# Optimization experiments

Measured on AMD Instinct MI355X. Metric: run time of the kernel, lower is better.

Reference implementation:

```python
import jax, jax.numpy as jnp
import numpy as np

RMS_EPS = 1e-6


def setup_inputs() -> dict:
    key = jax.random.key(0)
    ks = jax.random.split(key, 6)
    B, S, D, F, E = 4, 2048, 1024, 4096, 8
    scale = 0.02
    return {
        "hidden_states": jax.random.normal(ks[0], (B, S, D), dtype=jnp.float32),
        "norm_weight": jnp.ones((D,), dtype=jnp.float32),
        "gate_w": jax.random.normal(ks[1], (E, D), dtype=jnp.float32) * scale,
        "w1": jax.random.normal(ks[2], (E, D, F), dtype=jnp.float32) * scale,
        "w3": jax.random.normal(ks[3], (E, D, F), dtype=jnp.float32) * scale,
        "w2": jax.random.normal(ks[4], (E, F, D), dtype=jnp.float32) * scale,
        "top_k": 2,
    }


def reference(hidden_states, norm_weight, gate_w, w1, w3, w2, top_k):
    B, S, D = hidden_states.shape
    E = gate_w.shape[0]
    # norm_fn: RMSNorm (pre-MoE norm in Mixtral block)
    x = hidden_states * jax.lax.rsqrt(jnp.mean(jnp.square(hidden_states), axis=-1, keepdims=True) + RMS_EPS)
    x = (x * norm_weight).reshape(-1, D)  # [T, D], T = B*S
    # router
    router_logits = jnp.einsum('td,ed->te', x, gate_w)  # [T, E]
    routing = jax.nn.softmax(router_logits.astype(jnp.float32), axis=-1)
    top_w, top_idx = jax.lax.top_k(routing, top_k)  # [T, k]
    top_w = top_w / jnp.sum(top_w, axis=-1, keepdims=True)
    top_w = top_w.astype(x.dtype)
    # dense-masked expert combine: tokens not routed to expert e get weight 0,
    # mathematically identical to the gather/scatter loop in the original.
    out = jnp.zeros_like(x)
    for e in range(E):  # fixed small loop over experts
        w_e = jnp.sum(jnp.where(top_idx == e, top_w, 0.0), axis=-1)  # [T]
        h = jax.nn.silu(x @ w1[e]) * (x @ w3[e])  # [T, F] SwiGLU expert
        out = out + w_e[:, None] * (h @ w2[e])
    return out.reshape(B, S, D), router_logits
```

## Files before the change

kernel.cpp:

```cpp
#include <hip/hip_runtime.h>
#include <hip/hip_bf16.h>

#define T_TOK 8192
#define D_DIM 1024
#define F_DIM 4096
#define E_NUM 8

typedef short s16x8 __attribute__((ext_vector_type(8)));
typedef float f32x4 __attribute__((ext_vector_type(4)));
typedef unsigned short u16x8 __attribute__((ext_vector_type(8)));

__device__ __forceinline__ unsigned short f2bf(float f) {
  union { float f; unsigned int u; } v; v.f = f;
  unsigned int u = v.u;
  return (unsigned short)((u + 0x7FFFu + ((u >> 16) & 1u)) >> 16);
}

__device__ __forceinline__ void async16(const void* g, void* l) {
  __builtin_amdgcn_global_load_lds((const __attribute__((address_space(1))) void*)g,
                                   (__attribute__((address_space(3))) void*)l, 16, 0, 0);
}

__global__ __launch_bounds__(256) void prepass_kernel(
    const float* __restrict__ hs, const float* __restrict__ nw,
    const float* __restrict__ gw, const float* __restrict__ w1,
    const float* __restrict__ w3, const float* __restrict__ w2,
    unsigned short* __restrict__ xb, unsigned short* __restrict__ w13t,
    unsigned short* __restrict__ w2t, float* __restrict__ logits_out,
    int* __restrict__ cnt, int* __restrict__ ilist, float* __restrict__ wlist) {
  __shared__ unsigned short tileS[64][72];
  __shared__ float red[4];
  __shared__ float pl[4][8];
  int bx = blockIdx.x;
  int tid = threadIdx.x;
  if (bx < 24576) {
    int tensor = bx >> 13;
    int e = (bx >> 10) & 7;
    int tl = bx & 1023;
    const float* src; int C, tr, tc;
    if (tensor == 0) {
      src = w1 + (size_t)e * D_DIM * F_DIM; C = F_DIM; tr = tl >> 6; tc = tl & 63;
    } else if (tensor == 1) {
      src = w3 + (size_t)e * D_DIM * F_DIM; C = F_DIM; tr = tl >> 6; tc = tl & 63;
    } else {
      src = w2 + (size_t)e * F_DIM * D_DIM; C = D_DIM; tr = tl >> 4; tc = tl & 15;
    }
    int r0 = tr * 64, c0 = tc * 64;
    int rr = tid >> 4, ccb = (tid & 15) * 4;
#pragma unroll
    for (int i = 0; i < 4; ++i) {
      int r = rr + i * 16;
      float4 v = *(const float4*)(src + (size_t)(r0 + r) * C + c0 + ccb);
      tileS[ccb + 0][r] = f2bf(v.x);
      tileS[ccb + 1][r] = f2bf(v.y);
      tileS[ccb + 2][r] = f2bf(v.z);
      tileS[ccb + 3][r] = f2bf(v.w);
    }
    __syncthreads();
    int row = tid >> 2, col = (tid & 3) * 16;
    unsigned short* dp;
    if (tensor < 2) {
      int f = c0 + row;
      int prow = ((f >> 5) * 64) + (f & 31) + (tensor == 1 ? 32 : 0);
      dp = w13t + ((size_t)e * 8192 + prow) * D_DIM + r0 + col;
    } else {
      dp = w2t + ((size_t)e * D_DIM + c0 + row) * F_DIM + r0 + col;
    }
    u16x8 v0, v1;
#pragma unroll
    for (int j = 0; j < 8; ++j) { v0[j] = tileS[row][col + j]; v1[j] = tileS[row][col + 8 + j]; }
    *(u16x8*)dp = v0;
    *(u16x8*)(dp + 8) = v1;
  } else {
    int t = bx - 24576;
    int lane = tid & 63, wid = tid >> 6;
    float4 v = ((const float4*)(hs + (size_t)t * D_DIM))[tid];
    float ss = v.x * v.x + v.y * v.y + v.z * v.z + v.w * v.w;
#pragma unroll
    for (int o = 32; o > 0; o >>= 1) ss += __shfl_xor(ss, o);
    if (lane == 0) red[wid] = ss;
    __syncthreads();
    float ms = (red[0] + red[1] + red[2] + red[3]) * (1.0f / 1024.0f);
    float rs = rsqrtf(ms + 1e-6f);
    float4 wv = ((const float4*)nw)[tid];
    float x0 = v.x * rs * wv.x, x1 = v.y * rs * wv.y;
    float x2 = v.z * rs * wv.z, x3 = v.w * rs * wv.w;
    ((ushort4*)(xb + (size_t)t * D_DIM))[tid] =
        make_ushort4(f2bf(x0), f2bf(x1), f2bf(x2), f2bf(x3));
    float p[8];
#pragma unroll
    for (int e = 0; e < 8; ++e) {
      float4 g = ((const float4*)(gw + (size_t)e * D_DIM))[tid];
      p[e] = x0 * g.x + x1 * g.y + x2 * g.z + x3 * g.w;
    }
#pragma unroll
    for (int e = 0; e < 8; ++e) {
#pragma unroll
      for (int o = 32; o > 0; o >>= 1) p[e] += __shfl_xor(p[e], o);
    }
    if (lane == 0) {
#pragma unroll
      for (int e = 0; e < 8; ++e) pl[wid][e] = p[e];
    }
    __syncthreads();
    if (tid == 0) {
      float l[8];
#pragma unroll
      for (int e = 0; e < 8; ++e) {
        l[e] = pl[0][e] + pl[1][e] + pl[2][e] + pl[3][e];
        logits_out[(size_t)t * 8 + e] = l[e];
      }
      int i0 = 0; float b0 = l[0];
#pragma unroll
      for (int e = 1; e < 8; ++e) if (l[e] > b0) { b0 = l[e]; i0 = e; }
      int i1 = (i0 == 0) ? 1 : 0; float b1 = l[i1];
#pragma unroll
      for (int e = 0; e < 8; ++e) if (e != i0 && l[e] > b1) { b1 = l[e]; i1 = e; }
      float wa = 1.0f / (1.0f + __expf(b1 - b0));
      float wb = 1.0f / (1.0f + __expf(b0 - b1));
      int p0 = atomicAdd(&cnt[i0], 1);
      ilist[i0 * T_TOK + p0] = t * 2;     wlist[i0 * T_TOK + p0] = wa;
      int p1 = atomicAdd(&cnt[i1], 1);
      ilist[i1 * T_TOK + p1] = t * 2 + 1; wlist[i1 * T_TOK + p1] = wb;
    }
  }
}

__global__ __launch_bounds__(512, 2) void gemm1_kernel(
    const unsigned short* __restrict__ xb, const unsigned short* __restrict__ w13t,
    unsigned short* __restrict__ H, const int* __restrict__ cnt,
    const int* __restrict__ ilist) {
  int flat = blockIdx.x;
  int e = flat & 7;
  int widx = flat >> 3;
  int ne = cnt[e];
  int art = (ne + 255) >> 8;
  if (widx >= (art << 5)) return;
  int rt = widx % art;
  int ft = widx / art;
  int r0 = rt * 256;
  int hbase = 0;
#pragma unroll
  for (int j = 0; j < E_NUM; ++j) hbase += (j < e) ? cnt[j] : 0;
  __shared__ __align__(16) unsigned short As[3 * 8192];
  __shared__ __align__(16) unsigned short Bs[3 * 8192];
  __shared__ int toks[256];
  int tid = threadIdx.x, lane = tid & 63, w = tid >> 6;
  if (tid < 256) toks[tid] = ilist[e * T_TOK + min(r0 + tid, ne - 1)];
  __syncthreads();
  const unsigned short* bpanel = w13t + ((size_t)e * 8192 + ft * 256) * D_DIM;
  int sr0 = tid >> 2, sr1 = sr0 + 128;
  int ch0 = (((tid & 3) ^ ((sr0 >> 1) & 3)) * 8);
  int ch1 = (((tid & 3) ^ ((sr1 >> 1) & 3)) * 8);
  const unsigned short* ap0 = xb + (size_t)(toks[sr0] >> 1) * D_DIM + ch0;
  const unsigned short* ap1 = xb + (size_t)(toks[sr1] >> 1) * D_DIM + ch1;
  const unsigned short* bp0 = bpanel + (size_t)sr0 * D_DIM + ch0;
  const unsigned short* bp1 = bpanel + (size_t)sr1 * D_DIM + ch1;
  int d0 = (sr0 * 32) + (tid & 3) * 8;
  int d1 = d0 + 4096;
  int wr = w >> 2, wc = w & 3;
  int lr = lane & 15, lc = lane >> 4;
  int aoff[8], boff[4];
#pragma unroll
  for (int m = 0; m < 8; ++m) {
    int row = wr * 128 + m * 16 + lr;
    aoff[m] = row * 32 + ((lc ^ ((row >> 1) & 3)) * 8);
  }
#pragma unroll
  for (int n = 0; n < 4; ++n) {
    int row = wc * 64 + n * 16 + lr;
    boff[n] = row * 32 + ((lc ^ ((row >> 1) & 3)) * 8);
  }
  f32x4 acc[8][4] = {};
  async16(ap0, &As[d0]); async16(ap1, &As[d1]);
  async16(bp0, &Bs[d0]); async16(bp1, &Bs[d1]);
  async16(ap0 + 32, &As[8192 + d0]); async16(ap1 + 32, &As[8192 + d1]);
  async16(bp0 + 32, &Bs[8192 + d0]); async16(bp1 + 32, &Bs[8192 + d1]);

#define G1_STEP(T_, BUF_, VMC_, DOST_)                                          \
  {                                                                             \
    asm volatile("s_waitcnt vmcnt(" VMC_ ")" ::: "memory");                     \
    __builtin_amdgcn_s_barrier();                                               \
    const unsigned short* Ab = &As[(BUF_) * 8192];                              \
    const unsigned short* Bb = &Bs[(BUF_) * 8192];                              \
    s16x8 a[8], b[4];                                                           \
    if (DOST_) {                                   \
      int nk = ((T_) + 2) * 32;                                                 \
      async16(ap0 + nk, &As[(((BUF_) + 2) % 3) * 8192 + d0]);                   \
      async16(ap1 + nk, &As[(((BUF_) + 2) % 3) * 8192 + d1]);                   \
    }                                                                           \
    _Pragma("unroll") for (int m = 0; m < 4; ++m)                               \
        a[m] = *(const s16x8*)(Ab + aoff[m]);                                   \
    _Pragma("unroll") for (int n = 0; n < 4; ++n)                               \
        b[n] = *(const s16x8*)(Bb + boff[n]);                                   \
    __builtin_amdgcn_s_setprio(1);                                              \
    _Pragma("unroll") for (int m = 0; m < 4; ++m)                               \
        _Pragma("unroll") for (int n = 0; n < 4; ++n)                           \
            acc[m][n] = __builtin_amdgcn_mfma_f32_16x16x32_bf16(                \
                a[m], b[n], acc[m][n], 0, 0, 0);                                \
    __builtin_amdgcn_s_setprio(0);                                              \
    if (DOST_) {                                   \
      int nk = ((T_) + 2) * 32;                                                 \
      async16(bp0 + nk, &Bs[(((BUF_) + 2) % 3) * 8192 + d0]);                   \
      async16(bp1 + nk, &Bs[(((BUF_) + 2) % 3) * 8192 + d1]);                   \
    }                                                                           \
    _Pragma("unroll") for (int m = 4; m < 8; ++m)                               \
        a[m] = *(const s16x8*)(Ab + aoff[m]);                                   \
    __builtin_amdgcn_s_setprio(1);                                              \
    _Pragma("unroll") for (int m = 4; m < 8; ++m)                               \
        _Pragma("unroll") for (int n = 0; n < 4; ++n)                           \
            acc[m][n] = __builtin_amdgcn_mfma_f32_16x16x32_bf16(                \
                a[m], b[n], acc[m][n], 0, 0, 0);                                \
    __builtin_amdgcn_s_setprio(0);                                              \
  }

  for (int tb = 0; tb < 30; tb += 3) {
    G1_STEP(tb, 0, "4", 1)
    G1_STEP(tb + 1, 1, "4", 1)
    G1_STEP(tb + 2, 2, "4", 1)
  }
  G1_STEP(30, 0, "4", 0)
  G1_STEP(31, 1, "0", 0)
#undef G1_STEP

  int g4 = lane >> 4, cl = lane & 15;
  int fbase = (4 * ft + wc) * 32;
#pragma unroll
  for (int m = 0; m < 8; ++m) {
#pragma unroll
    for (int j = 0; j < 4; ++j) {
      int rloc = wr * 128 + m * 16 + g4 * 4 + j;
      if (r0 + rloc < ne) {
        unsigned short* hp = H + (size_t)(hbase + r0 + rloc) * F_DIM + fbase + cl;
#pragma unroll
        for (int n = 0; n < 2; ++n) {
          float c1 = acc[m][n][j], c3 = acc[m][n + 2][j];
          float h = c1 / (1.0f + __expf(-c1)) * c3;
          hp[n * 16] = f2bf(h);
        }
      }
    }
  }
}

__global__ __launch_bounds__(512, 2) void gemm2_kernel(
    const unsigned short* __restrict__ H, const unsigned short* __restrict__ w2t,
    const int* __restrict__ cnt, const int* __restrict__ ilist,
    const float* __restrict__ wlist, float* __restrict__ P) {
  int flat = blockIdx.x;
  int e = flat & 7;
  int widx = flat >> 3;
  int ne = cnt[e];
  int art = (ne + 255) >> 8;
  if (widx >= (art << 2)) return;
  int nt = widx & 3;
  int rt = widx >> 2;
  int r0 = rt * 256;
  int hbase = 0;
#pragma unroll
  for (int j = 0; j < E_NUM; ++j) hbase += (j < e) ? cnt[j] : 0;
  __shared__ __align__(16) unsigned short As[3 * 8192];
  __shared__ __align__(16) unsigned short Bs[3 * 8192];
  __shared__ int toks[256];
  __shared__ float wts[256];
  int tid = threadIdx.x, lane = tid & 63, w = tid >> 6;
  if (tid < 256) {
    int idx = e * T_TOK + min(r0 + tid, ne - 1);
    toks[tid] = ilist[idx];
    wts[tid] = wlist[idx];
  }
  __syncthreads();
  const unsigned short* bpanel = w2t + ((size_t)e * D_DIM + nt * 256) * F_DIM;
  int sr0 = tid >> 2, sr1 = sr0 + 128;
  int ch0 = (((tid & 3) ^ ((sr0 >> 1) & 3)) * 8);
  int ch1 = (((tid & 3) ^ ((sr1 >> 1) & 3)) * 8);
  const unsigned short* ap0 = H + (size_t)(hbase + min(r0 + sr0, ne - 1)) * F_DIM + ch0;
  const unsigned short* ap1 = H + (size_t)(hbase + min(r0 + sr1, ne - 1)) * F_DIM + ch1;
  const unsigned short* bp0 = bpanel + (size_t)sr0 * F_DIM + ch0;
  const unsigned short* bp1 = bpanel + (size_t)sr1 * F_DIM + ch1;
  int d0 = (sr0 * 32) + (tid & 3) * 8;
  int d1 = d0 + 4096;
  int wr = w >> 2, wc = w & 3;
  int lr = lane & 15, lc = lane >> 4;
  int aoff[8], boff[4];
#pragma unroll
  for (int m = 0; m < 8; ++m) {
    int row = wr * 128 + m * 16 + lr;
    aoff[m] = row * 32 + ((lc ^ ((row >> 1) & 3)) * 8);
  }
#pragma unroll
  for (int n = 0; n < 4; ++n) {
    int row = wc * 64 + n * 16 + lr;
    boff[n] = row * 32 + ((lc ^ ((row >> 1) & 3)) * 8);
  }
  f32x4 acc[8][4] = {};
  async16(ap0, &As[d0]); async16(ap1, &As[d1]);
  async16(bp0, &Bs[d0]); async16(bp1, &Bs[d1]);
  async16(ap0 + 32, &As[8192 + d0]); async16(ap1 + 32, &As[8192 + d1]);
  async16(bp0 + 32, &Bs[8192 + d0]); async16(bp1 + 32, &Bs[8192 + d1]);

#define G2_STEP(T_, BUF_, VMC_, DOST_)                                          \
  {                                                                             \
    asm volatile("s_waitcnt vmcnt(" VMC_ ")" ::: "memory");                     \
    __builtin_amdgcn_s_barrier();                                               \
    const unsigned short* Ab = &As[(BUF_) * 8192];                              \
    const unsigned short* Bb = &Bs[(BUF_) * 8192];                              \
    s16x8 a[8], b[4];                                                           \
    if (DOST_) {                                                                \
      int nk = ((T_) + 2) * 32;                                                 \
      async16(ap0 + nk, &As[(((BUF_) + 2) % 3) * 8192 + d0]);                   \
      async16(ap1 + nk, &As[(((BUF_) + 2) % 3) * 8192 + d1]);                   \
    }                                                                           \
    _Pragma("unroll") for (int m = 0; m < 4; ++m)                               \
        a[m] = *(const s16x8*)(Ab + aoff[m]);                                   \
    _Pragma("unroll") for (int n = 0; n < 4; ++n)                               \
        b[n] = *(const s16x8*)(Bb + boff[n]);                                   \
    __builtin_amdgcn_s_setprio(1);                                              \
    _Pragma("unroll") for (int m = 0; m < 4; ++m)                               \
        _Pragma("unroll") for (int n = 0; n < 4; ++n)                           \
            acc[m][n] = __builtin_amdgcn_mfma_f32_16x16x32_bf16(                \
                a[m], b[n], acc[m][n], 0, 0, 0);                                \
    __builtin_amdgcn_s_setprio(0);                                              \
    if (DOST_) {                                                                \
      int nk = ((T_) + 2) * 32;                                                 \
      async16(bp0 + nk, &Bs[(((BUF_) + 2) % 3) * 8192 + d0]);                   \
      async16(bp1 + nk, &Bs[(((BUF_) + 2) % 3) * 8192 + d1]);                   \
    }                                                                           \
    _Pragma("unroll") for (int m = 4; m < 8; ++m)                               \
        a[m] = *(const s16x8*)(Ab + aoff[m]);                                   \
    __builtin_amdgcn_s_setprio(1);                                              \
    _Pragma("unroll") for (int m = 4; m < 8; ++m)                               \
        _Pragma("unroll") for (int n = 0; n < 4; ++n)                           \
            acc[m][n] = __builtin_amdgcn_mfma_f32_16x16x32_bf16(                \
                a[m], b[n], acc[m][n], 0, 0, 0);                                \
    __builtin_amdgcn_s_setprio(0);                                              \
  }

  for (int tb = 0; tb < 126; tb += 3) {
    G2_STEP(tb, 0, "4", 1)
    G2_STEP(tb + 1, 1, "4", 1)
    G2_STEP(tb + 2, 2, "4", 1)
  }
  G2_STEP(126, 0, "4", 0)
  G2_STEP(127, 1, "0", 0)
#undef G2_STEP

  int g4 = lane >> 4, cl = lane & 15;
#pragma unroll
  for (int m = 0; m < 8; ++m) {
#pragma unroll
    for (int j = 0; j < 4; ++j) {
      int rloc = wr * 128 + m * 16 + g4 * 4 + j;
      if (r0 + rloc < ne) {
        int slot = toks[rloc];
        float ww = wts[rloc];
        float* pp = P + (size_t)slot * D_DIM + nt * 256 + wc * 64 + cl;
#pragma unroll
        for (int n = 0; n < 4; ++n)
          pp[n * 16] = ww * acc[m][n][j];
      }
    }
  }
}

__global__ __launch_bounds__(256) void combine_kernel(
    const float* __restrict__ P, float* __restrict__ out) {
  int i = blockIdx.x * 256 + threadIdx.x;
#pragma unroll
  for (int k = 0; k < 4; ++k) {
    int idx = i + k * 524288;
    int t = idx >> 8, c = idx & 255;
    float4 a = ((const float4*)P)[(size_t)(t * 2) * 256 + c];
    float4 b = ((const float4*)P)[(size_t)(t * 2 + 1) * 256 + c];
    float4 o;
    o.x = a.x + b.x; o.y = a.y + b.y; o.z = a.z + b.z; o.w = a.w + b.w;
    ((float4*)out)[idx] = o;
  }
}

extern "C" void kernel_launch(void* const* d_in, const int* in_sizes, int n_in,
                              void* d_out, int out_size, void* d_ws, size_t ws_size,
                              hipStream_t stream) {
  const float* hs = (const float*)d_in[0];
  const float* nw = (const float*)d_in[1];
  const float* gw = (const float*)d_in[2];
  const float* w1 = (const float*)d_in[3];
  const float* w3 = (const float*)d_in[4];
  const float* w2 = (const float*)d_in[5];
  float* out = (float*)d_out;
  float* logits_out = out + (size_t)T_TOK * D_DIM;

  char* ws = (char*)d_ws;
  unsigned short* xb   = (unsigned short*)(ws);
  unsigned short* w13t = (unsigned short*)(ws + 16777216ull);
  unsigned short* w2t  = (unsigned short*)(ws + 150994944ull);
  unsigned short* H    = (unsigned short*)(ws + 218103808ull);
  float* P = (float*)(ws + 16777216ull);
  int*   ilist = (int*)(ws + 352321536ull);
  float* wlist = (float*)(ws + 352583680ull);
  int*   cnt   = (int*)(ws + 352845824ull);

  hipMemsetAsync(cnt, 0, E_NUM * sizeof(int), stream);
  prepass_kernel<<<24576 + T_TOK, 256, 0, stream>>>(
      hs, nw, gw, w1, w3, w2, xb, w13t, w2t, logits_out, cnt, ilist, wlist);
  gemm1_kernel<<<E_NUM * 32 * 32, 512, 0, stream>>>(xb, w13t, H, cnt, ilist);
  gemm2_kernel<<<E_NUM * 32 * 4, 512, 0, stream>>>(H, w2t, cnt, ilist, wlist, P);
  combine_kernel<<<2048, 256, 0, stream>>>(P, out);
}
```

Measured before the change: 816.9 us.

## Move w2 bf16 transpose into idle gemm1 blocks to overlap with GEMM

The prepass kernel no longer converts and transposes w2. That work now runs in the gemm1 blocks that have no expert tile to process: each idle block handles two 64x64 w2 tiles, staged in its As shared buffer. The aim is to take this memory-bound conversion off the serial prepass and overlap it with the gemm1 matrix math. It relies on there always being at least 4096 idle blocks, which holds given the bound on per-expert row tiles. The idle blocks still reserve the full gemm1 shared memory.

```diff
diff --git a/kernel.cpp b/kernel.cpp
--- a/kernel.cpp
+++ b/kernel.cpp
@@ -24,33 +24,26 @@
 __global__ __launch_bounds__(256) void prepass_kernel(
     const float* __restrict__ hs, const float* __restrict__ nw,
     const float* __restrict__ gw, const float* __restrict__ w1,
-    const float* __restrict__ w3, const float* __restrict__ w2,
-    unsigned short* __restrict__ xb, unsigned short* __restrict__ w13t,
-    unsigned short* __restrict__ w2t, float* __restrict__ logits_out,
+    const float* __restrict__ w3, unsigned short* __restrict__ xb,
+    unsigned short* __restrict__ w13t, float* __restrict__ logits_out,
     int* __restrict__ cnt, int* __restrict__ ilist, float* __restrict__ wlist) {
   __shared__ unsigned short tileS[64][72];
   __shared__ float red[4];
   __shared__ float pl[4][8];
   int bx = blockIdx.x;
   int tid = threadIdx.x;
-  if (bx < 24576) {
+  if (bx < 16384) {
     int tensor = bx >> 13;
     int e = (bx >> 10) & 7;
     int tl = bx & 1023;
-    const float* src; int C, tr, tc;
-    if (tensor == 0) {
-      src = w1 + (size_t)e * D_DIM * F_DIM; C = F_DIM; tr = tl >> 6; tc = tl & 63;
-    } else if (tensor == 1) {
-      src = w3 + (size_t)e * D_DIM * F_DIM; C = F_DIM; tr = tl >> 6; tc = tl & 63;
-    } else {
-      src = w2 + (size_t)e * F_DIM * D_DIM; C = D_DIM; tr = tl >> 4; tc = tl & 15;
-    }
+    const float* src = (tensor == 0 ? w1 : w3) + (size_t)e * D_DIM * F_DIM;
+    int tr = tl >> 6, tc = tl & 63;
     int r0 = tr * 64, c0 = tc * 64;
     int rr = tid >> 4, ccb = (tid & 15) * 4;
 #pragma unroll
     for (int i = 0; i < 4; ++i) {
       int r = rr + i * 16;
-      float4 v = *(const float4*)(src + (size_t)(r0 + r) * C + c0 + ccb);
+      float4 v = *(const float4*)(src + (size_t)(r0 + r) * F_DIM + c0 + ccb);
       tileS[ccb + 0][r] = f2bf(v.x);
       tileS[ccb + 1][r] = f2bf(v.y);
       tileS[ccb + 2][r] = f2bf(v.z);
@@ -58,21 +51,16 @@
     }
     __syncthreads();
     int row = tid >> 2, col = (tid & 3) * 16;
-    unsigned short* dp;
-    if (tensor < 2) {
-      int f = c0 + row;
-      int prow = ((f >> 5) * 64) + (f & 31) + (tensor == 1 ? 32 : 0);
-      dp = w13t + ((size_t)e * 8192 + prow) * D_DIM + r0 + col;
-    } else {
-      dp = w2t + ((size_t)e * D_DIM + c0 + row) * F_DIM + r0 + col;
-    }
+    int f = c0 + row;
+    int prow = ((f >> 5) * 64) + (f & 31) + (tensor == 1 ? 32 : 0);
+    unsigned short* dp = w13t + ((size_t)e * 8192 + prow) * D_DIM + r0 + col;
     u16x8 v0, v1;
 #pragma unroll
     for (int j = 0; j < 8; ++j) { v0[j] = tileS[row][col + j]; v1[j] = tileS[row][col + 8 + j]; }
     *(u16x8*)dp = v0;
     *(u16x8*)(dp + 8) = v1;
   } else {
-    int t = bx - 24576;
+    int t = bx - 16384;
     int lane = tid & 63, wid = tid >> 6;
     float4 v = ((const float4*)(hs + (size_t)t * D_DIM))[tid];
     float ss = v.x * v.x + v.y * v.y + v.z * v.z + v.w * v.w;
@@ -129,23 +117,59 @@
 __global__ __launch_bounds__(512, 2) void gemm1_kernel(
     const unsigned short* __restrict__ xb, const unsigned short* __restrict__ w13t,
     unsigned short* __restrict__ H, const int* __restrict__ cnt,
-    const int* __restrict__ ilist) {
+    const int* __restrict__ ilist, const float* __restrict__ w2,
+    unsigned short* __restrict__ w2t) {
   int flat = blockIdx.x;
   int e = flat & 7;
   int widx = flat >> 3;
   int ne = cnt[e];
   int art = (ne + 255) >> 8;
-  if (widx >= (art << 5)) return;
+  int tid = threadIdx.x, lane = tid & 63, w = tid >> 6;
+  __shared__ __align__(16) unsigned short As[3 * 8192];
+  __shared__ __align__(16) unsigned short Bs[3 * 8192];
+  __shared__ int toks[256];
+  if (widx >= (art << 5)) {
+    int idle_before = 0;
+#pragma unroll
+    for (int j = 0; j < E_NUM; ++j) {
+      int aj = (cnt[j] + 255) >> 8;
+      idle_before += (j < e) ? (1024 - (aj << 5)) : 0;
+    }
+    int my_idle = idle_before + (widx - (art << 5));
+    if (my_idle >= 4096) return;
+    int h = tid >> 8, tid2 = tid & 255;
+    unsigned short* ts = (unsigned short*)As + h * 4608;
+    int tileIdx = my_idle * 2 + h;
+    int e2 = tileIdx >> 10, tl = tileIdx & 1023;
+    int tr = tl >> 4, tc = tl & 15;
+    const float* src = w2 + (size_t)e2 * F_DIM * D_DIM;
+    int r0 = tr * 64, c0 = tc * 64;
+    int rr = tid2 >> 4, ccb = (tid2 & 15) * 4;
+#pragma unroll
+    for (int i = 0; i < 4; ++i) {
+      int r = rr + i * 16;
+      float4 v = *(const float4*)(src + (size_t)(r0 + r) * D_DIM + c0 + ccb);
+      ts[(ccb + 0) * 72 + r] = f2bf(v.x);
+      ts[(ccb + 1) * 72 + r] = f2bf(v.y);
+      ts[(ccb + 2) * 72 + r] = f2bf(v.z);
+      ts[(ccb + 3) * 72 + r] = f2bf(v.w);
+    }
+    __syncthreads();
+    int row = tid2 >> 2, col = (tid2 & 3) * 16;
+    unsigned short* dp = w2t + ((size_t)e2 * D_DIM + c0 + row) * F_DIM + r0 + col;
+    u16x8 v0, v1;
+#pragma unroll
+    for (int j = 0; j < 8; ++j) { v0[j] = ts[row * 72 + col + j]; v1[j] = ts[row * 72 + col + 8 + j]; }
+    *(u16x8*)dp = v0;
+    *(u16x8*)(dp + 8) = v1;
+    return;
+  }
   int rt = widx % art;
   int ft = widx / art;
   int r0 = rt * 256;
   int hbase = 0;
 #pragma unroll
   for (int j = 0; j < E_NUM; ++j) hbase += (j < e) ? cnt[j] : 0;
-  __shared__ __align__(16) unsigned short As[3 * 8192];
-  __shared__ __align__(16) unsigned short Bs[3 * 8192];
-  __shared__ int toks[256];
-  int tid = threadIdx.x, lane = tid & 63, w = tid >> 6;
   if (tid < 256) toks[tid] = ilist[e * T_TOK + min(r0 + tid, ne - 1)];
   __syncthreads();
   const unsigned short* bpanel = w13t + ((size_t)e * 8192 + ft * 256) * D_DIM;
@@ -401,9 +425,9 @@
   int*   cnt   = (int*)(ws + 352845824ull);
 
   hipMemsetAsync(cnt, 0, E_NUM * sizeof(int), stream);
-  prepass_kernel<<<24576 + T_TOK, 256, 0, stream>>>(
-      hs, nw, gw, w1, w3, w2, xb, w13t, w2t, logits_out, cnt, ilist, wlist);
-  gemm1_kernel<<<E_NUM * 32 * 32, 512, 0, stream>>>(xb, w13t, H, cnt, ilist);
+  prepass_kernel<<<16384 + T_TOK, 256, 0, stream>>>(
+      hs, nw, gw, w1, w3, xb, w13t, logits_out, cnt, ilist, wlist);
+  gemm1_kernel<<<E_NUM * 32 * 32, 512, 0, stream>>>(xb, w13t, H, cnt, ilist, w2, w2t);
   gemm2_kernel<<<E_NUM * 32 * 4, 512, 0, stream>>>(H, w2t, cnt, ilist, wlist, P);
   combine_kernel<<<2048, 256, 0, stream>>>(P, out);
 }
```

New measurement: 834.9 us. 2.2% more time.

## Retile gemm2 to 128x256 blocks with 256 threads and move barrier to step end

Applied to the files above, without the earlier changes.

The down-projection GEMM now uses 128-row token tiles with 256 threads (4 waves in a 2x2 grid, each computing 64x128), doubling the grid to cover the smaller tiles. The pipeline issues all six next-stage loads up front and moves the wait/barrier to the end of each step, with a prologue wait. This targets the padding waste on the last partial row tile per expert and raises block count for better CU fill with variable expert sizes. In exchange it re-reads the W2 panel twice as often per token and gives less A reuse per block.

```diff
diff --git a/kernel.cpp b/kernel.cpp
--- a/kernel.cpp
+++ b/kernel.cpp
@@ -243,7 +243,7 @@
   }
 }
 
-__global__ __launch_bounds__(512, 2) void gemm2_kernel(
+__global__ __launch_bounds__(256, 2) void gemm2_kernel(
     const unsigned short* __restrict__ H, const unsigned short* __restrict__ w2t,
     const int* __restrict__ cnt, const int* __restrict__ ilist,
     const float* __restrict__ wlist, float* __restrict__ P) {
@@ -251,112 +251,116 @@
   int e = flat & 7;
   int widx = flat >> 3;
   int ne = cnt[e];
-  int art = (ne + 255) >> 8;
+  int art = (ne + 127) >> 7;
   if (widx >= (art << 2)) return;
   int nt = widx & 3;
   int rt = widx >> 2;
-  int r0 = rt * 256;
+  int r0 = rt * 128;
   int hbase = 0;
 #pragma unroll
   for (int j = 0; j < E_NUM; ++j) hbase += (j < e) ? cnt[j] : 0;
-  __shared__ __align__(16) unsigned short As[3 * 8192];
+  __shared__ __align__(16) unsigned short As[3 * 4096];
   __shared__ __align__(16) unsigned short Bs[3 * 8192];
-  __shared__ int toks[256];
-  __shared__ float wts[256];
+  __shared__ int toks[128];
+  __shared__ float wts[128];
   int tid = threadIdx.x, lane = tid & 63, w = tid >> 6;
-  if (tid < 256) {
+  if (tid < 128) {
     int idx = e * T_TOK + min(r0 + tid, ne - 1);
     toks[tid] = ilist[idx];
     wts[tid] = wlist[idx];
   }
   __syncthreads();
   const unsigned short* bpanel = w2t + ((size_t)e * D_DIM + nt * 256) * F_DIM;
-  int sr0 = tid >> 2, sr1 = sr0 + 128;
-  int ch0 = (((tid & 3) ^ ((sr0 >> 1) & 3)) * 8);
-  int ch1 = (((tid & 3) ^ ((sr1 >> 1) & 3)) * 8);
-  const unsigned short* ap0 = H + (size_t)(hbase + min(r0 + sr0, ne - 1)) * F_DIM + ch0;
-  const unsigned short* ap1 = H + (size_t)(hbase + min(r0 + sr1, ne - 1)) * F_DIM + ch1;
-  const unsigned short* bp0 = bpanel + (size_t)sr0 * F_DIM + ch0;
-  const unsigned short* bp1 = bpanel + (size_t)sr1 * F_DIM + ch1;
-  int d0 = (sr0 * 32) + (tid & 3) * 8;
-  int d1 = d0 + 4096;
-  int wr = w >> 2, wc = w & 3;
+  int ar0 = tid >> 2, ar1 = ar0 + 64;
+  int ca0 = (((tid & 3) ^ ((ar0 >> 1) & 3)) * 8);
+  int ca1 = (((tid & 3) ^ ((ar1 >> 1) & 3)) * 8);
+  const unsigned short* ap0 = H + (size_t)(hbase + min(r0 + ar0, ne - 1)) * F_DIM + ca0;
+  const unsigned short* ap1 = H + (size_t)(hbase + min(r0 + ar1, ne - 1)) * F_DIM + ca1;
+  int da0 = tid * 8;
+  int da1 = 2048 + tid * 8;
+  int br0 = tid >> 2, br1 = br0 + 64, br2 = br0 + 128, br3 = br0 + 192;
+  int cb0 = (((tid & 3) ^ ((br0 >> 1) & 3)) * 8);
+  int cb1 = (((tid & 3) ^ ((br1 >> 1) & 3)) * 8);
+  int cb2 = (((tid & 3) ^ ((br2 >> 1) & 3)) * 8);
+  int cb3 = (((tid & 3) ^ ((br3 >> 1) & 3)) * 8);
+  const unsigned short* bp0 = bpanel + (size_t)br0 * F_DIM + cb0;
+  const unsigned short* bp1 = bpanel + (size_t)br1 * F_DIM + cb1;
+  const unsigned short* bp2 = bpanel + (size_t)br2 * F_DIM + cb2;
+  const unsigned short* bp3 = bpanel + (size_t)br3 * F_DIM + cb3;
+  int db0 = tid * 8, db1 = 2048 + tid * 8, db2 = 4096 + tid * 8, db3 = 6144 + tid * 8;
+  int wr = w >> 1, wc = w & 1;
   int lr = lane & 15, lc = lane >> 4;
-  int aoff[8], boff[4];
-#pragma unroll
-  for (int m = 0; m < 8; ++m) {
-    int row = wr * 128 + m * 16 + lr;
+  int aoff[4], boff[8];
+#pragma unroll
+  for (int m = 0; m < 4; ++m) {
+    int row = wr * 64 + m * 16 + lr;
     aoff[m] = row * 32 + ((lc ^ ((row >> 1) & 3)) * 8);
   }
 #pragma unroll
-  for (int n = 0; n < 4; ++n) {
-    int row = wc * 64 + n * 16 + lr;
+  for (int n = 0; n < 8; ++n) {
+    int row = wc * 128 + n * 16 + lr;
     boff[n] = row * 32 + ((lc ^ ((row >> 1) & 3)) * 8);
   }
-  f32x4 acc[8][4] = {};
-  async16(ap0, &As[d0]); async16(ap1, &As[d1]);
-  async16(bp0, &Bs[d0]); async16(bp1, &Bs[d1]);
-  async16(ap0 + 32, &As[8192 + d0]); async16(ap1 + 32, &As[8192 + d1]);
-  async16(bp0 + 32, &Bs[8192 + d0]); async16(bp1 + 32, &Bs[8192 + d1]);
+  f32x4 acc[4][8] = {};
+  async16(ap0, &As[da0]); async16(ap1, &As[da1]);
+  async16(bp0, &Bs[db0]); async16(bp1, &Bs[db1]);
+  async16(bp2, &Bs[db2]); async16(bp3, &Bs[db3]);
+  async16(ap0 + 32, &As[4096 + da0]); async16(ap1 + 32, &As[4096 + da1]);
+  async16(bp0 + 32, &Bs[8192 + db0]); async16(bp1 + 32, &Bs[8192 + db1]);
+  async16(bp2 + 32, &Bs[8192 + db2]); async16(bp3 + 32, &Bs[8192 + db3]);
+  asm volatile("s_waitcnt vmcnt(6)" ::: "memory");
+  __builtin_amdgcn_s_barrier();
 
 #define G2_STEP(T_, BUF_, VMC_, DOST_)                                          \
   {                                                                             \
-    asm volatile("s_waitcnt vmcnt(" VMC_ ")" ::: "memory");                     \
-    __builtin_amdgcn_s_barrier();                                               \
-    const unsigned short* Ab = &As[(BUF_) * 8192];                              \
+    const unsigned short* Ab = &As[(BUF_) * 4096];                              \
     const unsigned short* Bb = &Bs[(BUF_) * 8192];                              \
-    s16x8 a[8], b[4];                                                           \
+    s16x8 a[4], b[8];                                                           \
     if (DOST_) {                                                                \
       int nk = ((T_) + 2) * 32;                                                 \
-      async16(ap0 + nk, &As[(((BUF_) + 2) % 3) * 8192 + d0]);                   \
-      async16(ap1 + nk, &As[(((BUF_) + 2) % 3) * 8192 + d1]);                   \
+      int nb = ((BUF_) + 2) % 3;                                                \
+      async16(ap0 + nk, &As[nb * 4096 + da0]);                                  \
+      async16(ap1 + nk, &As[nb * 4096 + da1]);                                  \
+      async16(bp0 + nk, &Bs[nb * 8192 + db0]);                                  \
+      async16(bp1 + nk, &Bs[nb * 8192 + db1]);                                  \
+      async16(bp2 + nk, &Bs[nb * 8192 + db2]);                                  \
+      async16(bp3 + nk, &Bs[nb * 8192 + db3]);                                  \
     }                                                                           \
     _Pragma("unroll") for (int m = 0; m < 4; ++m)                               \
         a[m] = *(const s16x8*)(Ab + aoff[m]);                                   \
-    _Pragma("unroll") for (int n = 0; n < 4; ++n)                               \
+    _Pragma("unroll") for (int n = 0; n < 8; ++n)                               \
         b[n] = *(const s16x8*)(Bb + boff[n]);                                   \
     __builtin_amdgcn_s_setprio(1);                                              \
     _Pragma("unroll") for (int m = 0; m < 4; ++m)                               \
-        _Pragma("unroll") for (int n = 0; n < 4; ++n)                           \
+        _Pragma("unroll") for (int n = 0; n < 8; ++n)                           \
             acc[m][n] = __builtin_amdgcn_mfma_f32_16x16x32_bf16(                \
                 a[m], b[n], acc[m][n], 0, 0, 0);                                \
     __builtin_amdgcn_s_setprio(0);                                              \
-    if (DOST_) {                                                                \
-      int nk = ((T_) + 2) * 32;                                                 \
-      async16(bp0 + nk, &Bs[(((BUF_) + 2) % 3) * 8192 + d0]);                   \
-      async16(bp1 + nk, &Bs[(((BUF_) + 2) % 3) * 8192 + d1]);                   \
-    }                                                                           \
-    _Pragma("unroll") for (int m = 4; m < 8; ++m)                               \
-        a[m] = *(const s16x8*)(Ab + aoff[m]);                                   \
-    __builtin_amdgcn_s_setprio(1);                                              \
-    _Pragma("unroll") for (int m = 4; m < 8; ++m)                               \
-        _Pragma("unroll") for (int n = 0; n < 4; ++n)                           \
-            acc[m][n] = __builtin_amdgcn_mfma_f32_16x16x32_bf16(                \
-                a[m], b[n], acc[m][n], 0, 0, 0);                                \
-    __builtin_amdgcn_s_setprio(0);                                              \
+    asm volatile("s_waitcnt vmcnt(" VMC_ ")" ::: "memory");                     \
+    __builtin_amdgcn_s_barrier();                                               \
   }
 
   for (int tb = 0; tb < 126; tb += 3) {
-    G2_STEP(tb, 0, "4", 1)
-    G2_STEP(tb + 1, 1, "4", 1)
-    G2_STEP(tb + 2, 2, "4", 1)
-  }
-  G2_STEP(126, 0, "4", 0)
+    G2_STEP(tb, 0, "6", 1)
+    G2_STEP(tb + 1, 1, "6", 1)
+    G2_STEP(tb + 2, 2, "6", 1)
+  }
+  G2_STEP(126, 0, "0", 0)
   G2_STEP(127, 1, "0", 0)
 #undef G2_STEP
 
   int g4 = lane >> 4, cl = lane & 15;
 #pragma unroll
-  for (int m = 0; m < 8; ++m) {
+  for (int m = 0; m < 4; ++m) {
 #pragma unroll
     for (int j = 0; j < 4; ++j) {
-      int rloc = wr * 128 + m * 16 + g4 * 4 + j;
+      int rloc = wr * 64 + m * 16 + g4 * 4 + j;
       if (r0 + rloc < ne) {
         int slot = toks[rloc];
         float ww = wts[rloc];
-        float* pp = P + (size_t)slot * D_DIM + nt * 256 + wc * 64 + cl;
-#pragma unroll
-        for (int n = 0; n < 4; ++n)
+        float* pp = P + (size_t)slot * D_DIM + nt * 256 + wc * 128 + cl;
+#pragma unroll
+        for (int n = 0; n < 8; ++n)
           pp[n * 16] = ww * acc[m][n][j];
       }
     }
@@ -404,6 +408,6 @@
   prepass_kernel<<<24576 + T_TOK, 256, 0, stream>>>(
       hs, nw, gw, w1, w3, w2, xb, w13t, w2t, logits_out, cnt, ilist, wlist);
   gemm1_kernel<<<E_NUM * 32 * 32, 512, 0, stream>>>(xb, w13t, H, cnt, ilist);
-  gemm2_kernel<<<E_NUM * 32 * 4, 512, 0, stream>>>(H, w2t, cnt, ilist, wlist, P);
+  gemm2_kernel<<<E_NUM * 64 * 4, 256, 0, stream>>>(H, w2t, cnt, ilist, wlist, P);
   combine_kernel<<<2048, 256, 0, stream>>>(P, out);
 }
```

New measurement: 831.9 us. Within noise of the previous version (+1.8%).
